# Performance work log

Measured on AMD Instinct MI355X. Metric: run time of the kernel, lower is better.

Reference implementation:

```python
import jax, jax.numpy as jnp
import numpy as np

S = 2048          # total tokens (prefill, batch folded into seq dim)
H = 32            # num query heads
HKV = 8           # num kv heads (GQA)
G = H // HKV      # query heads per kv head
D = 128           # head_dim
SCALE = D ** -0.5 # flex_attention default scale
DIFF_BS = 32      # diffusion block size for the block mask


def setup_inputs() -> dict:
    key = jax.random.key(0)
    k1, k2, k3 = jax.random.split(key, 3)
    q = jax.random.normal(k1, (S, H * D), dtype=jnp.float32)
    k = jax.random.normal(k2, (S, HKV * D), dtype=jnp.float32)
    v = jax.random.normal(k3, (S, HKV * D), dtype=jnp.float32)
    # diffusion block-causal mask: token i attends to all tokens in diffusion
    # blocks up to and including its own block (matches attn_metadata.block_mask
    # semantics fed into dllm_block_mask / flex_attention)
    blk = jnp.arange(S) // DIFF_BS
    block_mask = blk[:, None] >= blk[None, :]  # [S, S] bool
    return {"q": q, "k": k, "v": v, "block_mask": block_mask}


def reference(q, k, v, block_mask):
    # q: [S, H*D]; k, v: [S, HKV*D]; block_mask: [S, S] bool
    qh = q.reshape(S, HKV, G, D)   # group query heads by shared kv head (enable_gqa)
    kh = k.reshape(S, HKV, D)
    vh = v.reshape(S, HKV, D)
    # scores: [HKV, G, S_q, S_k]
    scores = jnp.einsum('qhgd,khd->hgqk', qh, kh) * SCALE
    neg = jnp.finfo(scores.dtype).min
    scores = jnp.where(block_mask[None, None, :, :], scores, neg)
    p = jax.nn.softmax(scores, axis=-1)
    o = jnp.einsum('hgqk,khd->qhgd', p, vh)  # [S, HKV, G, D]
    # prefill epilogue: rearrange '1 h s d -> s (h d)'
    return o.reshape(S, H * D)
```

## Files before the change

kernel.cpp:

```cpp
#include <hip/hip_runtime.h>
#include <hip/hip_bf16.h>

typedef __attribute__((ext_vector_type(8)))  short short8;
typedef __attribute__((ext_vector_type(16))) float f32x16;
typedef unsigned short u16;
typedef unsigned int   u32;

__device__ __forceinline__ u16 f2b(float f){
    __hip_bfloat16 h = __float2bfloat16(f);
    u16 u; __builtin_memcpy(&u, &h, 2); return u;
}
__device__ __forceinline__ u32 pk2(float lo, float hi){
    return (u32)f2b(lo) | ((u32)f2b(hi) << 16);
}
__device__ __forceinline__ float b2f(u16 u){
    u32 w = ((u32)u) << 16; float f; __builtin_memcpy(&f, &w, 4); return f;
}

#define PART_STRIDE 8448

template<bool SPLIT>
__global__ __launch_bounds__(256, 2)
void dllm_attn(const float* __restrict__ Qg, const float* __restrict__ Kg,
               const float* __restrict__ Vg, float* __restrict__ Og,
               char* __restrict__ Wg)
{
    __shared__ alignas(16) char kl[64 * 256];
    __shared__ alignas(16) char vl[128 * 128];

    const int bid = blockIdx.x;
    const int kh  = bid & 7;
    int tq, ci, uu = 0;
    if (SPLIT){
        uu = 159 - (bid >> 3);
        if (uu < 16)      { tq = uu; ci = 0; }
        else if (uu < 48) { const int x = uu - 16; tq = 16 + (x >> 1); ci = x & 1; }
        else if (uu < 96) { const int x = uu - 48; const int d3 = x / 3; tq = 32 + d3; ci = x - 3 * d3; }
        else              { const int x = uu - 96; tq = 48 + (x >> 2); ci = x & 3; }
    } else { tq = 63 - (bid >> 3); ci = 0; }
    const int q0   = tq << 5;
    const int nvis = q0 + 32;
    const int ntt  = (tq + 2) >> 1;
    const int t0   = SPLIT ? (ci << 3) : 0;
    const int t1   = SPLIT ? min(t0 + 8, ntt) : ntt;
    const int nch  = SPLIT ? ((tq >> 4) + 1) : 1;

    const int tid = threadIdx.x;
    const int wv  = tid >> 6;
    const int ln  = tid & 63;
    const int lq  = ln & 31;
    const int hi  = ln >> 5;
    const int swz = (ln & 7) << 4;
    const int h   = (kh << 2) + wv;

    const float QS = 0.088388347648318447f * 1.4426950408889634f;
    short8 qf[8];
    {
        const float* qp = Qg + (size_t)(q0 + lq) * 4096 + h * 128 + hi * 8;
        #pragma unroll
        for (int ds = 0; ds < 8; ++ds){
            const float4 a = *reinterpret_cast<const float4*>(qp + ds * 16);
            const float4 b = *reinterpret_cast<const float4*>(qp + ds * 16 + 4);
            qf[ds] = __builtin_bit_cast(short8,
                make_uint4(pk2(a.x * QS, a.y * QS), pk2(a.z * QS, a.w * QS),
                           pk2(b.x * QS, b.y * QS), pk2(b.z * QS, b.w * QS)));
        }
    }

    f32x16 oa[4];
    #pragma unroll
    for (int i = 0; i < 4; ++i)
        #pragma unroll
        for (int j = 0; j < 16; ++j) oa[i][j] = 0.f;
    float mR = -1e30f, lR = 0.f;

    const int sr = tid >> 2;
    const int sc = (tid & 3) << 5;

    for (int t = t0; t < t1; ++t){
        const int kv0 = t << 6;
        const bool full = (kv0 + 64) <= nvis;

        __syncthreads();
        {
            const float* kp = Kg + (size_t)(kv0 + sr) * 1024 + (kh << 7) + sc;
            #pragma unroll
            for (int w = 0; w < 4; ++w){
                const float4 a = *reinterpret_cast<const float4*>(kp + w * 8);
                const float4 b = *reinterpret_cast<const float4*>(kp + w * 8 + 4);
                const uint4 pkd = make_uint4(pk2(a.x,a.y), pk2(a.z,a.w),
                                             pk2(b.x,b.y), pk2(b.z,b.w));
                const int byte = sr * 256 + (((sc << 1) + (w << 4)) ^ ((sr & 7) << 4));
                *reinterpret_cast<uint4*>(&kl[byte]) = pkd;
            }
            const float* vp = Vg + (size_t)(kv0 + sr) * 1024 + (kh << 7) + sc;
            #pragma unroll
            for (int w = 0; w < 8; ++w){
                const float4 a = *reinterpret_cast<const float4*>(vp + w * 4);
                const float vv[4] = {a.x, a.y, a.z, a.w};
                #pragma unroll
                for (int e = 0; e < 4; ++e){
                    const int row = sc + (w << 2) + e;
                    const int byte = (row << 7) + ((sr << 1) ^ ((row & 7) << 4));
                    *reinterpret_cast<u16*>(&vl[byte]) = f2b(vv[e]);
                }
            }
        }
        __syncthreads();

        f32x16 s0, s1;
        #pragma unroll
        for (int i = 0; i < 16; ++i){ s0[i] = 0.f; s1[i] = 0.f; }
        #pragma unroll
        for (int ds = 0; ds < 8; ++ds){
            const short8 a0 = *reinterpret_cast<const short8*>(
                &kl[lq * 256 + (((ds << 5) + (hi << 4)) ^ swz)]);
            s0 = __builtin_amdgcn_mfma_f32_32x32x16_bf16(a0, qf[ds], s0, 0, 0, 0);
        }
        if (full){
            #pragma unroll
            for (int ds = 0; ds < 8; ++ds){
                const short8 a1 = *reinterpret_cast<const short8*>(
                    &kl[(32 + lq) * 256 + (((ds << 5) + (hi << 4)) ^ swz)]);
                s1 = __builtin_amdgcn_mfma_f32_32x32x16_bf16(a1, qf[ds], s1, 0, 0, 0);
            }
        }

        float p0[16], p1[16];
        float mx = -1e30f;
        #pragma unroll
        for (int r = 0; r < 16; ++r){ p0[r] = s0[r]; mx = fmaxf(mx, s0[r]); }
        if (full){
            #pragma unroll
            for (int r = 0; r < 16; ++r){ p1[r] = s1[r]; mx = fmaxf(mx, s1[r]); }
        }
        mx = fmaxf(mx, __shfl_xor(mx, 32, 64));
        const float mn = fmaxf(mR, mx);
        const float cf = __builtin_exp2f(mR - mn);
        mR = mn;
        float ps = 0.f;
        #pragma unroll
        for (int r = 0; r < 16; ++r){ p0[r] = __builtin_exp2f(p0[r] - mn); ps += p0[r]; }
        if (full){
            #pragma unroll
            for (int r = 0; r < 16; ++r){ p1[r] = __builtin_exp2f(p1[r] - mn); ps += p1[r]; }
        }
        ps += __shfl_xor(ps, 32, 64);
        lR = lR * cf + ps;
        #pragma unroll
        for (int i = 0; i < 4; ++i)
            #pragma unroll
            for (int j = 0; j < 16; ++j) oa[i][j] *= cf;

        u32 pw0[8], px0[8], pw1[8], px1[8];
        #pragma unroll
        for (int rr = 0; rr < 8; ++rr){
            pw0[rr] = pk2(p0[2*rr], p0[2*rr+1]);
            px0[rr] = (u32)__shfl_xor((int)pw0[rr], 32, 64);
        }
        if (full){
            #pragma unroll
            for (int rr = 0; rr < 8; ++rr){
                pw1[rr] = pk2(p1[2*rr], p1[2*rr+1]);
                px1[rr] = (u32)__shfl_xor((int)pw1[rr], 32, 64);
            }
        }

        short8 pf[4];
        #pragma unroll
        for (int ks = 0; ks < 4; ++ks){
            if (ks < 2 || full){
                const u32* pwt = (ks >> 1) ? pw1 : pw0;
                const u32* pxt = (ks >> 1) ? px1 : px0;
                u32 wb[4];
                #pragma unroll
                for (int w = 0; w < 4; ++w){
                    const int b = (w & 1) + ((ks & 1) << 2);
                    const u32 own = hi ? pwt[b + 2] : pwt[b];
                    const u32 oth = hi ? pxt[b + 2] : pxt[b];
                    wb[w] = (hi == (w >> 1)) ? own : oth;
                }
                pf[ks] = __builtin_bit_cast(short8, make_uint4(wb[0], wb[1], wb[2], wb[3]));
            }
        }

        #pragma unroll
        for (int dt = 0; dt < 4; ++dt){
            #pragma unroll
            for (int ks = 0; ks < 4; ++ks){
                if (ks < 2 || full){
                    const short8 vf = *reinterpret_cast<const short8*>(
                        &vl[((dt << 5) + lq) * 128 + (((ks << 5) + (hi << 4)) ^ swz)]);
                    oa[dt] = __builtin_amdgcn_mfma_f32_32x32x16_bf16(vf, pf[ks], oa[dt], 0, 0, 0);
                }
            }
        }
    }

    if (!SPLIT || nch == 1){
        const float rl = 1.f / lR;
        float* op = Og + (size_t)(q0 + lq) * 4096 + (h << 7) + (hi << 2);
        #pragma unroll
        for (int dt = 0; dt < 4; ++dt){
            #pragma unroll
            for (int g2 = 0; g2 < 4; ++g2){
                float4 w4;
                w4.x = oa[dt][4*g2 + 0] * rl;
                w4.y = oa[dt][4*g2 + 1] * rl;
                w4.z = oa[dt][4*g2 + 2] * rl;
                w4.w = oa[dt][4*g2 + 3] * rl;
                *reinterpret_cast<float4*>(op + (dt << 5) + (g2 << 3)) = w4;
            }
        }
    } else {
        const int pu = ((kh * 144 + (uu - 16)) << 2) + wv;
        char* base = Wg + (size_t)pu * PART_STRIDE;
        #pragma unroll
        for (int i = 0; i < 8; ++i){
            const int e0 = i * 8;
            uint4 w4;
            w4.x = pk2(oa[(e0+0)>>4][(e0+0)&15], oa[(e0+1)>>4][(e0+1)&15]);
            w4.y = pk2(oa[(e0+2)>>4][(e0+2)&15], oa[(e0+3)>>4][(e0+3)&15]);
            w4.z = pk2(oa[(e0+4)>>4][(e0+4)&15], oa[(e0+5)>>4][(e0+5)&15]);
            w4.w = pk2(oa[(e0+6)>>4][(e0+6)&15], oa[(e0+7)>>4][(e0+7)&15]);
            *reinterpret_cast<uint4*>(base + ln * 128 + i * 16) = w4;
        }
        if (hi == 0){
            *reinterpret_cast<float*>(base + 8192 + lq * 4) = mR;
            *reinterpret_cast<float*>(base + 8320 + lq * 4) = lR;
        }
    }
}

__global__ __launch_bounds__(256, 2)
void dllm_merge(float* __restrict__ Og, const char* __restrict__ Wg)
{
    const int b  = blockIdx.x;
    const int h  = b & 31;
    const int tq = 16 + (b >> 5);
    const int kh = h >> 2, wv = h & 3;
    const int nch = (tq >> 4) + 1;
    int ub;
    if (tq < 32)      ub = 16 + ((tq - 16) << 1);
    else if (tq < 48) ub = 48 + (tq - 32) * 3;
    else              ub = 96 + ((tq - 48) << 2);

    const int tid = threadIdx.x;
    const int q   = tid >> 3;
    const int s   = tid & 7;

    const char* bases[4];
    float mv[4], lv[4];
    float M = -1e30f;
    #pragma unroll
    for (int c = 0; c < 4; ++c){
        if (c < nch){
            bases[c] = Wg + (size_t)(((kh * 144 + (ub - 16 + c)) << 2) + wv) * PART_STRIDE;
            mv[c] = *reinterpret_cast<const float*>(bases[c] + 8192 + q * 4);
            lv[c] = *reinterpret_cast<const float*>(bases[c] + 8320 + q * 4);
            M = fmaxf(M, mv[c]);
        }
    }
    uint4 wlo[4], whi[4];
    #pragma unroll
    for (int c = 0; c < 4; ++c){
        if (c < nch){
            wlo[c] = *reinterpret_cast<const uint4*>(bases[c] + q * 128 + s * 16);
            whi[c] = *reinterpret_cast<const uint4*>(bases[c] + (q + 32) * 128 + s * 16);
        }
    }
    float wsum = 0.f;
    float acc[16];
    #pragma unroll
    for (int e = 0; e < 16; ++e) acc[e] = 0.f;
    #pragma unroll
    for (int c = 0; c < 4; ++c){
        if (c < nch){
            const float w = __builtin_exp2f(mv[c] - M);
            wsum += lv[c] * w;
            const u32 wl[4] = {wlo[c].x, wlo[c].y, wlo[c].z, wlo[c].w};
            const u32 wh[4] = {whi[c].x, whi[c].y, whi[c].z, whi[c].w};
            #pragma unroll
            for (int k = 0; k < 4; ++k){
                const int dl = ((k & 1) << 1) + ((k >> 1) << 3);
                acc[dl + 0] += b2f((u16)(wl[k] & 0xffffu)) * w;
                acc[dl + 1] += b2f((u16)(wl[k] >> 16)) * w;
                acc[dl + 4] += b2f((u16)(wh[k] & 0xffffu)) * w;
                acc[dl + 5] += b2f((u16)(wh[k] >> 16)) * w;
            }
        }
    }
    const float rl = 1.f / wsum;
    float* op = Og + (size_t)((tq << 5) + q) * 4096 + h * 128 + (s << 4);
    #pragma unroll
    for (int g = 0; g < 4; ++g){
        float4 v4;
        v4.x = acc[g*4 + 0] * rl;
        v4.y = acc[g*4 + 1] * rl;
        v4.z = acc[g*4 + 2] * rl;
        v4.w = acc[g*4 + 3] * rl;
        *reinterpret_cast<float4*>(op + (g << 2)) = v4;
    }
}

extern "C" void kernel_launch(void* const* d_in, const int* in_sizes, int n_in,
                              void* d_out, int out_size, void* d_ws, size_t ws_size,
                              hipStream_t stream) {
    const float* Q = (const float*)d_in[0];
    const float* K = (const float*)d_in[1];
    const float* V = (const float*)d_in[2];
    float* O = (float*)d_out;
    const size_t need = (size_t)4608 * PART_STRIDE;
    if (ws_size >= need){
        dllm_attn<true><<<dim3(1280), dim3(256), 0, stream>>>(Q, K, V, O, (char*)d_ws);
        dllm_merge<<<dim3(1536), dim3(256), 0, stream>>>(O, (const char*)d_ws);
    } else {
        dllm_attn<false><<<dim3(512), dim3(256), 0, stream>>>(Q, K, V, O, (char*)d_ws);
    }
}
```

Before: 228.2 us.

## Process 64 query rows per block with 8 waves sharing K/V tiles

```diff
diff --git a/kernel.cpp b/kernel.cpp
--- a/kernel.cpp
+++ b/kernel.cpp
@@ -20,7 +20,7 @@
 #define PART_STRIDE 8448
 
 template<bool SPLIT>
-__global__ __launch_bounds__(256, 2)
+__global__ __launch_bounds__(512, 2)
 void dllm_attn(const float* __restrict__ Qg, const float* __restrict__ Kg,
                const float* __restrict__ Vg, float* __restrict__ Og,
                char* __restrict__ Wg)
@@ -30,33 +30,35 @@
 
     const int bid = blockIdx.x;
     const int kh  = bid & 7;
-    int tq, ci, uu = 0;
+    int tq2, ci, uu = 0;
     if (SPLIT){
-        uu = 159 - (bid >> 3);
-        if (uu < 16)      { tq = uu; ci = 0; }
-        else if (uu < 48) { const int x = uu - 16; tq = 16 + (x >> 1); ci = x & 1; }
-        else if (uu < 96) { const int x = uu - 48; const int d3 = x / 3; tq = 32 + d3; ci = x - 3 * d3; }
-        else              { const int x = uu - 96; tq = 48 + (x >> 2); ci = x & 3; }
-    } else { tq = 63 - (bid >> 3); ci = 0; }
-    const int q0   = tq << 5;
-    const int nvis = q0 + 32;
-    const int ntt  = (tq + 2) >> 1;
-    const int t0   = SPLIT ? (ci << 3) : 0;
-    const int t1   = SPLIT ? min(t0 + 8, ntt) : ntt;
-    const int nch  = SPLIT ? ((tq >> 4) + 1) : 1;
+        uu = 79 - (bid >> 3);
+        if (uu < 8)       { tq2 = uu; ci = 0; }
+        else if (uu < 24) { const int x = uu - 8;  tq2 = 8  + (x >> 1); ci = x & 1; }
+        else if (uu < 48) { const int x = uu - 24; const int d3 = x / 3; tq2 = 16 + d3; ci = x - 3 * d3; }
+        else              { const int x = uu - 48; tq2 = 24 + (x >> 2); ci = x & 3; }
+    } else { tq2 = 31 - (bid >> 3); ci = 0; }
+    const int ntt = tq2 + 1;
+    const int t0  = SPLIT ? (ci << 3) : 0;
+    const int t1  = SPLIT ? min(t0 + 8, ntt) : ntt;
+    const int nch = SPLIT ? ((tq2 >> 3) + 1) : 1;
 
     const int tid = threadIdx.x;
     const int wv  = tid >> 6;
     const int ln  = tid & 63;
     const int lq  = ln & 31;
     const int hi  = ln >> 5;
-    const int swz = (ln & 7) << 4;
-    const int h   = (kh << 2) + wv;
+    const int swz = (lq & 7) << 4;
+    const int hgrp = wv & 3;
+    const int half = wv >> 2;
+    const int h   = (kh << 2) + hgrp;
+    const int qw0 = (tq2 << 6) + (half << 5);
+    const int nvis = qw0 + 32;
 
     const float QS = 0.088388347648318447f * 1.4426950408889634f;
     short8 qf[8];
     {
-        const float* qp = Qg + (size_t)(q0 + lq) * 4096 + h * 128 + hi * 8;
+        const float* qp = Qg + (size_t)(qw0 + lq) * 4096 + h * 128 + hi * 8;
         #pragma unroll
         for (int ds = 0; ds < 8; ++ds){
             const float4 a = *reinterpret_cast<const float4*>(qp + ds * 16);
@@ -74,8 +76,10 @@
         for (int j = 0; j < 16; ++j) oa[i][j] = 0.f;
     float mR = -1e30f, lR = 0.f;
 
-    const int sr = tid >> 2;
-    const int sc = (tid & 3) << 5;
+    const int krow = tid >> 3;
+    const int kdc  = tid & 7;
+    const int vk0  = wv << 3;
+    const int dA   = ln;
 
     for (int t = t0; t < t1; ++t){
         const int kv0 = t << 6;
@@ -83,34 +87,39 @@
 
         __syncthreads();
         {
-            const float* kp = Kg + (size_t)(kv0 + sr) * 1024 + (kh << 7) + sc;
-            #pragma unroll
-            for (int w = 0; w < 4; ++w){
-                const float4 a = *reinterpret_cast<const float4*>(kp + w * 8);
-                const float4 b = *reinterpret_cast<const float4*>(kp + w * 8 + 4);
-                const uint4 pkd = make_uint4(pk2(a.x,a.y), pk2(a.z,a.w),
-                                             pk2(b.x,b.y), pk2(b.z,b.w));
-                const int byte = sr * 256 + (((sc << 1) + (w << 4)) ^ ((sr & 7) << 4));
-                *reinterpret_cast<uint4*>(&kl[byte]) = pkd;
-            }
-            const float* vp = Vg + (size_t)(kv0 + sr) * 1024 + (kh << 7) + sc;
-            #pragma unroll
-            for (int w = 0; w < 8; ++w){
-                const float4 a = *reinterpret_cast<const float4*>(vp + w * 4);
-                const float vv[4] = {a.x, a.y, a.z, a.w};
-                #pragma unroll
-                for (int e = 0; e < 4; ++e){
-                    const int row = sc + (w << 2) + e;
-                    const int byte = (row << 7) + ((sr << 1) ^ ((row & 7) << 4));
-                    *reinterpret_cast<u16*>(&vl[byte]) = f2b(vv[e]);
-                }
-            }
+            const float* kp = Kg + (size_t)(kv0 + krow) * 1024 + (kh << 7) + (kdc << 4);
+            const float4 a = *reinterpret_cast<const float4*>(kp);
+            const float4 b = *reinterpret_cast<const float4*>(kp + 4);
+            const float4 c = *reinterpret_cast<const float4*>(kp + 8);
+            const float4 d = *reinterpret_cast<const float4*>(kp + 12);
+            const int kb = krow * 256 + (kdc << 5);
+            const int key = (krow & 7) << 4;
+            *reinterpret_cast<uint4*>(&kl[krow * 256 + ((kdc << 5) ^ key)]) =
+                make_uint4(pk2(a.x,a.y), pk2(a.z,a.w), pk2(b.x,b.y), pk2(b.z,b.w));
+            *reinterpret_cast<uint4*>(&kl[krow * 256 + (((kdc << 5) + 16) ^ key)]) =
+                make_uint4(pk2(c.x,c.y), pk2(c.z,c.w), pk2(d.x,d.y), pk2(d.z,d.w));
+            (void)kb;
+            const float* vp = Vg + (size_t)(kv0 + vk0) * 1024 + (kh << 7);
+            float va[8], vb[8];
+            #pragma unroll
+            for (int j = 0; j < 8; ++j){
+                va[j] = vp[j * 1024 + dA];
+                vb[j] = vp[j * 1024 + 64 + dA];
+            }
+            *reinterpret_cast<uint4*>(&vl[dA * 128 + ((vk0 << 1) ^ ((dA & 7) << 4))]) =
+                make_uint4(pk2(va[0],va[1]), pk2(va[2],va[3]),
+                           pk2(va[4],va[5]), pk2(va[6],va[7]));
+            const int dB = dA + 64;
+            *reinterpret_cast<uint4*>(&vl[dB * 128 + ((vk0 << 1) ^ ((dB & 7) << 4))]) =
+                make_uint4(pk2(vb[0],vb[1]), pk2(vb[2],vb[3]),
+                           pk2(vb[4],vb[5]), pk2(vb[6],vb[7]));
         }
         __syncthreads();
 
         f32x16 s0, s1;
         #pragma unroll
         for (int i = 0; i < 16; ++i){ s0[i] = 0.f; s1[i] = 0.f; }
+        __builtin_amdgcn_s_setprio(1);
         #pragma unroll
         for (int ds = 0; ds < 8; ++ds){
             const short8 a0 = *reinterpret_cast<const short8*>(
@@ -125,6 +134,7 @@
                 s1 = __builtin_amdgcn_mfma_f32_32x32x16_bf16(a1, qf[ds], s1, 0, 0, 0);
             }
         }
+        __builtin_amdgcn_s_setprio(0);
 
         float p0[16], p1[16];
         float mx = -1e30f;
@@ -184,6 +194,7 @@
             }
         }
 
+        __builtin_amdgcn_s_setprio(1);
         #pragma unroll
         for (int dt = 0; dt < 4; ++dt){
             #pragma unroll
@@ -195,11 +206,12 @@
                 }
             }
         }
+        __builtin_amdgcn_s_setprio(0);
     }
 
     if (!SPLIT || nch == 1){
         const float rl = 1.f / lR;
-        float* op = Og + (size_t)(q0 + lq) * 4096 + (h << 7) + (hi << 2);
+        float* op = Og + (size_t)(qw0 + lq) * 4096 + (h << 7) + (hi << 2);
         #pragma unroll
         for (int dt = 0; dt < 4; ++dt){
             #pragma unroll
@@ -213,7 +225,7 @@
             }
         }
     } else {
-        const int pu = ((kh * 144 + (uu - 16)) << 2) + wv;
+        const int pu = ((kh * 72 + (uu - 8)) << 3) + wv;
         char* base = Wg + (size_t)pu * PART_STRIDE;
         #pragma unroll
         for (int i = 0; i < 8; ++i){
@@ -235,15 +247,18 @@
 __global__ __launch_bounds__(256, 2)
 void dllm_merge(float* __restrict__ Og, const char* __restrict__ Wg)
 {
-    const int b  = blockIdx.x;
-    const int h  = b & 31;
-    const int tq = 16 + (b >> 5);
-    const int kh = h >> 2, wv = h & 3;
-    const int nch = (tq >> 4) + 1;
-    int ub;
-    if (tq < 32)      ub = 16 + ((tq - 16) << 1);
-    else if (tq < 48) ub = 48 + (tq - 32) * 3;
-    else              ub = 96 + ((tq - 48) << 2);
+    const int b    = blockIdx.x;
+    const int h    = b & 31;
+    const int r    = b >> 5;
+    const int tq2  = 8 + (r >> 1);
+    const int half = r & 1;
+    const int kh = h >> 2, hgrp = h & 3;
+    const int wvIdx = (half << 2) | hgrp;
+    const int nch = (tq2 >> 3) + 1;
+    int cb;
+    if (tq2 < 16)      cb = (tq2 - 8) << 1;
+    else if (tq2 < 24) cb = 16 + (tq2 - 16) * 3;
+    else               cb = 40 + ((tq2 - 24) << 2);
 
     const int tid = threadIdx.x;
     const int q   = tid >> 3;
@@ -255,7 +270,7 @@
     #pragma unroll
     for (int c = 0; c < 4; ++c){
         if (c < nch){
-            bases[c] = Wg + (size_t)(((kh * 144 + (ub - 16 + c)) << 2) + wv) * PART_STRIDE;
+            bases[c] = Wg + (size_t)(((kh * 72 + cb + c) << 3) + wvIdx) * PART_STRIDE;
             mv[c] = *reinterpret_cast<const float*>(bases[c] + 8192 + q * 4);
             lv[c] = *reinterpret_cast<const float*>(bases[c] + 8320 + q * 4);
             M = fmaxf(M, mv[c]);
@@ -291,7 +306,7 @@
         }
     }
     const float rl = 1.f / wsum;
-    float* op = Og + (size_t)((tq << 5) + q) * 4096 + h * 128 + (s << 4);
+    float* op = Og + (size_t)((tq2 << 6) + (half << 5) + q) * 4096 + h * 128 + (s << 4);
     #pragma unroll
     for (int g = 0; g < 4; ++g){
         float4 v4;
@@ -312,9 +327,9 @@
     float* O = (float*)d_out;
     const size_t need = (size_t)4608 * PART_STRIDE;
     if (ws_size >= need){
-        dllm_attn<true><<<dim3(1280), dim3(256), 0, stream>>>(Q, K, V, O, (char*)d_ws);
+        dllm_attn<true><<<dim3(640), dim3(512), 0, stream>>>(Q, K, V, O, (char*)d_ws);
         dllm_merge<<<dim3(1536), dim3(256), 0, stream>>>(O, (const char*)d_ws);
     } else {
-        dllm_attn<false><<<dim3(512), dim3(256), 0, stream>>>(Q, K, V, O, (char*)d_ws);
-    }
-}
+        dllm_attn<false><<<dim3(256), dim3(512), 0, stream>>>(Q, K, V, O, (char*)d_ws);
+    }
+}
```

New measurement: 211.5 us. -7.3%, faster.
